# Optimization experiments

Hardware: AMD Instinct MI355X
Metric: run time of the kernel (lower is better)

Reference implementation:

```python
import jax, jax.numpy as jnp
import numpy as np

PAD = 1
K = 3  # kernel_size


def conv2d(x, w, b):
    y = jax.lax.conv_general_dilated(
        x, w, window_strides=(1, 1), padding=((PAD, PAD), (PAD, PAD)),
        dimension_numbers=("NCHW", "OIHW", "NCHW"))
    return y + b[None, :, None, None]


def deform_conv2d(x, offset, weight, bias):
    # torchvision.ops.deform_conv2d semantics (stride=1, dilation=1, 1 offset group)
    B, C, H, W = x.shape
    O = weight.shape[0]
    K2 = K * K
    off = offset.reshape(B, K2, 2, H, W)  # [...,0]=dy, [...,1]=dx
    ky, kx = jnp.meshgrid(jnp.arange(K), jnp.arange(K), indexing="ij")
    ky = ky.reshape(K2).astype(x.dtype)
    kx = kx.reshape(K2).astype(x.dtype)
    hh = jnp.arange(H, dtype=x.dtype)
    ww = jnp.arange(W, dtype=x.dtype)
    # sampling coords, shape [B, K2, H, W]
    py = off[:, :, 0] + ky[None, :, None, None] + hh[None, None, :, None] - PAD
    px = off[:, :, 1] + kx[None, :, None, None] + ww[None, None, None, :] - PAD

    y0 = jnp.floor(py)
    x0 = jnp.floor(px)
    wy = (py - y0)[:, None]  # [B,1,K2,H,W]
    wx = (px - x0)[:, None]

    xf = x.reshape(B, C, H * W)

    def gather(iy, ix):
        valid = (iy >= 0) & (iy < H) & (ix >= 0) & (ix < W)
        iyc = jnp.clip(iy, 0, H - 1).astype(jnp.int32)
        ixc = jnp.clip(ix, 0, W - 1).astype(jnp.int32)
        idx = (iyc * W + ixc).reshape(B, 1, K2 * H * W)
        v = jnp.take_along_axis(xf, idx, axis=2).reshape(B, C, K2, H, W)
        return v * valid.reshape(B, 1, K2, H, W).astype(x.dtype)

    v00 = gather(y0, x0)
    v01 = gather(y0, x0 + 1)
    v10 = gather(y0 + 1, x0)
    v11 = gather(y0 + 1, x0 + 1)
    sampled = (v00 * (1 - wy) * (1 - wx) + v01 * (1 - wy) * wx
               + v10 * wy * (1 - wx) + v11 * wy * wx)  # [B,C,K2,H,W]
    out = jnp.einsum("bckhw,ock->bohw", sampled, weight.reshape(O, C, K2))
    return out + bias[None, :, None, None]


def setup_inputs() -> dict:
    key = jax.random.key(0)
    k1, k2, k3, k4, k5 = jax.random.split(key, 5)
    B, C, H, W = 4, 64, 192, 192
    O = 64
    x = jax.random.normal(k1, (B, C, H, W), dtype=jnp.float32)
    w_off = jax.random.normal(k2, (2 * K * K, C, K, K), dtype=jnp.float32) * 0.05
    b_off = jnp.zeros((2 * K * K,), dtype=jnp.float32)
    w_conv = jax.random.normal(k3, (O, C, K, K), dtype=jnp.float32) * (1.0 / np.sqrt(C * K * K))
    b_conv = jax.random.normal(k4, (O,), dtype=jnp.float32) * 0.01
    return {"x": x, "w_off": w_off, "b_off": b_off, "w_conv": w_conv, "b_conv": b_conv}


def reference(x, w_off, b_off, w_conv, b_conv):
    offset = conv2d(x, w_off, b_off)
    y = deform_conv2d(x, offset, w_conv, b_conv)
    return conv2d(y, w_conv, b_conv)  # module reuses self.conv on deform output
```

## Files before the change

### kernel.cpp

```cpp
#include <hip/hip_runtime.h>

constexpr int B = 4;
constexpr int C = 64;
constexpr int O = 64;
constexpr int OOFF = 18;
constexpr int H = 192;
constexpr int W = 192;

typedef __attribute__((ext_vector_type(8))) short short8;
typedef __attribute__((ext_vector_type(4))) float float4v;
typedef __attribute__((ext_vector_type(2))) float f32x2;
typedef __attribute__((ext_vector_type(2))) uint u32x2;
typedef __attribute__((ext_vector_type(2))) __bf16 bf16x2;

__device__ inline ushort f2bf(float f) {
  return __builtin_bit_cast(ushort, (__bf16)f);
}
__device__ inline uint pk2bf(float lo, float hi) {
  bf16x2 v;
  v.x = (__bf16)lo;
  v.y = (__bf16)hi;
  return __builtin_bit_cast(uint, v);
}
__device__ inline f32x2 upk(uint u) {
  u32x2 t;
  t.x = u << 16;
  t.y = u & 0xffff0000u;
  return __builtin_bit_cast(f32x2, t);
}

__global__ __launch_bounds__(256) void k_pre(const float* __restrict__ x,
                                             ushort* __restrict__ xtb,
                                             const float* __restrict__ w_conv,
                                             ushort* __restrict__ wBf,
                                             const float* __restrict__ w_off,
                                             ushort* __restrict__ wOf) {
  __shared__ float tile[64][17];
  const int bid = blockIdx.x;
  const int tid = threadIdx.x;
  if (bid < 9216) {
    const int w0 = (bid % 12) * 16;
    const int h = (bid / 12) % 192;
    const int b = bid / 2304;
    const int wl = tid & 15;
    const int c0 = tid >> 4;
#pragma unroll
    for (int r = 0; r < 4; ++r) {
      const int c = c0 + r * 16;
      tile[c][wl] = x[(((size_t)b * C + c) * H + h) * W + w0 + wl];
    }
    __syncthreads();
    const int c = tid & 63;
    const int qq = tid >> 6;
#pragma unroll
    for (int r = 0; r < 4; ++r) {
      const int wq = qq + r * 4;
      xtb[(((size_t)b * H + h) * W + w0 + wq) * C + c] = f2bf(tile[c][wq]);
    }
  } else if (bid < 9360) {
    const int i = (bid - 9216) * 256 + tid;
    const int j = i & 7;
    const int lane = (i >> 3) & 63;
    const int nt = (i >> 9) & 3;
    const int kstep = (i >> 11) & 1;
    const int kk = i >> 12;
    const int n = nt + 4 * (lane & 15);
    const int c = kstep * 32 + ((lane >> 4) & 3) * 8 + j;
    wBf[i] = f2bf(w_conv[((size_t)n * C + c) * 9 + kk]);
  } else {
    const int i = (bid - 9360) * 256 + tid;
    const int j = i & 7;
    const int lane = (i >> 3) & 63;
    const int nt = (i >> 9) & 1;
    const int ks = (i >> 10) & 1;
    const int kk = i >> 11;
    const int n = nt * 16 + (lane & 15);
    const int c = ks * 32 + ((lane >> 4) & 3) * 8 + j;
    wOf[i] = (n < OOFF) ? f2bf(w_off[((size_t)n * C + c) * 9 + kk]) : (ushort)0;
  }
}

__global__ __launch_bounds__(256) void k_conv_off_mfma(
    const ushort* __restrict__ xtb, const ushort* __restrict__ wOf,
    const float* __restrict__ b_off, float* __restrict__ offp) {
  const int w0 = blockIdx.x * 16;
  const int b = blockIdx.z;
  const int tid = threadIdx.x;
  const int wave = tid >> 6, lane = tid & 63;
  const int col = lane & 15, quad = lane >> 4;
  const int h0 = blockIdx.y * 8 + wave * 2;

  float4v acc[2][2];
#pragma unroll
  for (int mt = 0; mt < 2; ++mt)
#pragma unroll
    for (int nt = 0; nt < 2; ++nt) acc[mt][nt] = (float4v){0.f, 0.f, 0.f, 0.f};

  short8 bfr[2][2][2];
  short8 afr[2][2][2];

  auto load = [&](int kk, int pb) {
    const int ky = kk / 3, kx = kk % 3;
    const int ww = w0 + col + kx - 1;
    const bool wok = (unsigned)ww < (unsigned)W;
    const int wwc = min(max(ww, 0), W - 1);
#pragma unroll
    for (int ks = 0; ks < 2; ++ks)
#pragma unroll
      for (int nt = 0; nt < 2; ++nt)
        bfr[pb][ks][nt] = *(const short8*)&wOf[((((size_t)kk * 2 + ks) * 2 + nt) * 64 + lane) * 8];
#pragma unroll
    for (int mt = 0; mt < 2; ++mt) {
      const int hh = h0 + mt + ky - 1;
      const bool ok = wok && ((unsigned)hh < (unsigned)H);
      const int hhc = min(max(hh, 0), H - 1);
      const ushort* pa = xtb + (((size_t)b * H + hhc) * W + wwc) * C + quad * 8;
#pragma unroll
      for (int ks = 0; ks < 2; ++ks) {
        short8 v = (short8)0;
        if (ok) v = *(const short8*)(pa + ks * 32);
        afr[pb][mt][ks] = v;
      }
    }
  };

  load(0, 0);
#pragma unroll
  for (int kk = 0; kk < 9; ++kk) {
    const int pb = kk & 1;
    if (kk < 8) load(kk + 1, pb ^ 1);
#pragma unroll
    for (int ks = 0; ks < 2; ++ks)
#pragma unroll
      for (int mt = 0; mt < 2; ++mt)
#pragma unroll
        for (int nt = 0; nt < 2; ++nt)
          acc[mt][nt] = __builtin_amdgcn_mfma_f32_16x16x32_bf16(afr[pb][mt][ks], bfr[pb][ks][nt],
                                                                acc[mt][nt], 0, 0, 0);
  }

#pragma unroll
  for (int mt = 0; mt < 2; ++mt) {
    const int h = h0 + mt;
#pragma unroll
    for (int nt = 0; nt < 2; ++nt) {
      const int o = nt * 16 + col;
      if (o < OOFF) {
        const float bias = b_off[o];
#pragma unroll
        for (int r = 0; r < 4; ++r) {
          const int w = w0 + quad * 4 + r;
          offp[(((size_t)b * H + h) * W + w) * OOFF + o] = acc[mt][nt][r] + bias;
        }
      }
    }
  }
}

__global__ __launch_bounds__(256, 3) void k_deform_mfma(
    const ushort* __restrict__ xtb, const float* __restrict__ offp,
    const ushort* __restrict__ wBf, const float* __restrict__ b_conv,
    ushort* __restrict__ yt) {
  __shared__ ushort sA[2][2][4][64][8];

  const int bid = blockIdx.x;
  const int xcd = bid & 7;
  const int s = bid >> 3;
  const int b = xcd >> 1;
  const int half = xcd & 1;
  const int th = half * 12 + s / 24;
  const int tw = s % 24;
  const int h0 = th * 8, w0 = tw * 8;

  const int tid = threadIdx.x;
  const int wave = tid >> 6, lane = tid & 63;
  const int p = tid >> 2, qtr = tid & 3;
  const int prow = p >> 3, pcol = p & 7;
  const int h = h0 + prow, w = w0 + pcol;
  const int ks_w = qtr >> 1;
  const int q2 = (qtr & 1) * 2;

  const float* po = offp + ((size_t)(b * H + h) * W + w) * OOFF;
  float2 offv[9];
#pragma unroll
  for (int kk = 0; kk < 9; ++kk) offv[kk] = *(const float2*)(po + 2 * kk);

  const ushort* xb = xtb + (size_t)b * H * W * C + qtr * 16;

  uint4 G[2][8];
  float4 aw[2];

  auto issue = [&](int kk, int buf) {
    const float dy = offv[kk].x, dx = offv[kk].y;
    const int ky = kk / 3, kx = kk % 3;
    const float pyf = dy + (float)(ky + h - 1);
    const float pxf = dx + (float)(kx + w - 1);
    const float fy0 = floorf(pyf), fx0 = floorf(pxf);
    const float wy = pyf - fy0, wx = pxf - fx0;
    const int iy0 = (int)fy0, ix0 = (int)fx0;
    const int iy1 = iy0 + 1, ix1 = ix0 + 1;
    const bool vy0 = (unsigned)iy0 < (unsigned)H;
    const bool vy1 = (unsigned)iy1 < (unsigned)H;
    const bool vx0 = (unsigned)ix0 < (unsigned)W;
    const bool vx1 = (unsigned)ix1 < (unsigned)W;
    aw[buf].x = (vy0 && vx0) ? (1.f - wy) * (1.f - wx) : 0.f;
    aw[buf].y = (vy0 && vx1) ? (1.f - wy) * wx : 0.f;
    aw[buf].z = (vy1 && vx0) ? wy * (1.f - wx) : 0.f;
    aw[buf].w = (vy1 && vx1) ? wy * wx : 0.f;
    const int cy0 = min(max(iy0, 0), H - 1), cy1 = min(max(iy1, 0), H - 1);
    const int cx0 = min(max(ix0, 0), W - 1), cx1 = min(max(ix1, 0), W - 1);
    const uint4* p00 = (const uint4*)(xb + ((size_t)cy0 * W + cx0) * C);
    const uint4* p01 = (const uint4*)(xb + ((size_t)cy0 * W + cx1) * C);
    const uint4* p10 = (const uint4*)(xb + ((size_t)cy1 * W + cx0) * C);
    const uint4* p11 = (const uint4*)(xb + ((size_t)cy1 * W + cx1) * C);
    G[buf][0] = p00[0]; G[buf][1] = p00[1];
    G[buf][2] = p01[0]; G[buf][3] = p01[1];
    G[buf][4] = p10[0]; G[buf][5] = p10[1];
    G[buf][6] = p11[0]; G[buf][7] = p11[1];
  };

  float4v acc[4];
#pragma unroll
  for (int nt = 0; nt < 4; ++nt) acc[nt] = (float4v){0.f, 0.f, 0.f, 0.f};

  issue(0, 0);
#pragma unroll
  for (int kk = 0; kk < 9; ++kk) {
    const int buf = kk & 1;
    if (kk < 8) issue(kk + 1, buf ^ 1);

    const f32x2 a00 = {aw[buf].x, aw[buf].x};
    const f32x2 a01 = {aw[buf].y, aw[buf].y};
    const f32x2 a10 = {aw[buf].z, aw[buf].z};
    const f32x2 a11 = {aw[buf].w, aw[buf].w};
    uint pk[8];
#pragma unroll
    for (int i = 0; i < 8; ++i) {
      const uint u00 = ((const uint*)&G[buf][0])[i];
      const uint u01 = ((const uint*)&G[buf][2])[i];
      const uint u10 = ((const uint*)&G[buf][4])[i];
      const uint u11 = ((const uint*)&G[buf][6])[i];
      f32x2 sv = upk(u00) * a00 + upk(u01) * a01 + upk(u10) * a10 + upk(u11) * a11;
      pk[i] = pk2bf(sv.x, sv.y);
    }
    *(uint4*)&sA[buf][ks_w][p >> 4][(p & 15) | (q2 << 4)][0] = *(const uint4*)&pk[0];
    *(uint4*)&sA[buf][ks_w][p >> 4][(p & 15) | ((q2 + 1) << 4)][0] = *(const uint4*)&pk[4];
    __syncthreads();

#pragma unroll
    for (int ks = 0; ks < 2; ++ks) {
      const short8 a = *(const short8*)&sA[buf][ks][wave][lane][0];
#pragma unroll
      for (int nt = 0; nt < 4; ++nt) {
        const short8 bb = *(const short8*)&wBf[((((size_t)kk * 2 + ks) * 4 + nt) * 64 + lane) * 8];
        acc[nt] = __builtin_amdgcn_mfma_f32_16x16x32_bf16(a, bb, acc[nt], 0, 0, 0);
      }
    }
  }

  const int quad = lane >> 4, c16 = lane & 15;
  float bias[4];
#pragma unroll
  for (int nt = 0; nt < 4; ++nt) bias[nt] = b_conv[4 * c16 + nt];
#pragma unroll
  for (int r = 0; r < 4; ++r) {
    const int pp = wave * 16 + quad * 4 + r;
    const int hrow = h0 + (pp >> 3), wcol = w0 + (pp & 7);
    uint2 u;
    u.x = pk2bf(acc[0][r] + bias[0], acc[1][r] + bias[1]);
    u.y = pk2bf(acc[2][r] + bias[2], acc[3][r] + bias[3]);
    *(uint2*)&yt[((size_t)(b * H + hrow) * W + wcol) * C + 4 * c16] = u;
  }
}

__global__ __launch_bounds__(256) void k_conv_main_mfma(
    const ushort* __restrict__ yt, const ushort* __restrict__ wBf,
    const float* __restrict__ b_conv, float* __restrict__ out) {
  const int w0 = blockIdx.x * 16;
  const int b = blockIdx.z;
  const int tid = threadIdx.x;
  const int wave = tid >> 6, lane = tid & 63;
  const int col = lane & 15, quad = lane >> 4;
  const int h0 = blockIdx.y * 8 + wave * 2;

  float4v acc[2][4];
#pragma unroll
  for (int mt = 0; mt < 2; ++mt)
#pragma unroll
    for (int nt = 0; nt < 4; ++nt) acc[mt][nt] = (float4v){0.f, 0.f, 0.f, 0.f};

  short8 bfr[2][2][4];
  short8 afr[2][2][2];

  auto load = [&](int kk, int pb) {
    const int ky = kk / 3, kx = kk % 3;
    const int ww = w0 + col + kx - 1;
    const bool wok = (unsigned)ww < (unsigned)W;
    const int wwc = min(max(ww, 0), W - 1);
#pragma unroll
    for (int ks = 0; ks < 2; ++ks)
#pragma unroll
      for (int nt = 0; nt < 4; ++nt)
        bfr[pb][ks][nt] = *(const short8*)&wBf[((((size_t)kk * 2 + ks) * 4 + nt) * 64 + lane) * 8];
#pragma unroll
    for (int mt = 0; mt < 2; ++mt) {
      const int hh = h0 + mt + ky - 1;
      const bool ok = wok && ((unsigned)hh < (unsigned)H);
      const int hhc = min(max(hh, 0), H - 1);
      const ushort* pa = yt + (((size_t)b * H + hhc) * W + wwc) * C + quad * 8;
#pragma unroll
      for (int ks = 0; ks < 2; ++ks) {
        short8 v = (short8)0;
        if (ok) v = *(const short8*)(pa + ks * 32);
        afr[pb][mt][ks] = v;
      }
    }
  };

  load(0, 0);
#pragma unroll
  for (int kk = 0; kk < 9; ++kk) {
    const int pb = kk & 1;
    if (kk < 8) load(kk + 1, pb ^ 1);
#pragma unroll
    for (int ks = 0; ks < 2; ++ks)
#pragma unroll
      for (int mt = 0; mt < 2; ++mt)
#pragma unroll
        for (int nt = 0; nt < 4; ++nt)
          acc[mt][nt] = __builtin_amdgcn_mfma_f32_16x16x32_bf16(afr[pb][mt][ks], bfr[pb][ks][nt],
                                                                acc[mt][nt], 0, 0, 0);
  }

  float bias[4];
#pragma unroll
  for (int nt = 0; nt < 4; ++nt) bias[nt] = b_conv[4 * col + nt];
#pragma unroll
  for (int mt = 0; mt < 2; ++mt) {
    const int h = h0 + mt;
#pragma unroll
    for (int nt = 0; nt < 4; ++nt) {
      const int oc = 4 * col + nt;
      float4 v;
      v.x = acc[mt][nt][0] + bias[nt];
      v.y = acc[mt][nt][1] + bias[nt];
      v.z = acc[mt][nt][2] + bias[nt];
      v.w = acc[mt][nt][3] + bias[nt];
      *(float4*)&out[(((size_t)b * O + oc) * H + h) * W + w0 + quad * 4] = v;
    }
  }
}

extern "C" void kernel_launch(void* const* d_in, const int* in_sizes, int n_in,
                              void* d_out, int out_size, void* d_ws, size_t ws_size,
                              hipStream_t stream) {
  const float* x = (const float*)d_in[0];
  const float* w_off = (const float*)d_in[1];
  const float* b_off = (const float*)d_in[2];
  const float* w_conv = (const float*)d_in[3];
  const float* b_conv = (const float*)d_in[4];
  float* out = (float*)d_out;

  float* offp = (float*)d_ws;
  ushort* xtb = (ushort*)(offp + (size_t)B * H * W * OOFF);
  ushort* yt = xtb + (size_t)B * H * W * C;
  ushort* wBf = yt + (size_t)B * H * W * C;
  ushort* wOf = wBf + 36864;

  const dim3 blk(256);
  k_pre<<<dim3(9432), blk, 0, stream>>>(x, xtb, w_conv, wBf, w_off, wOf);
  k_conv_off_mfma<<<dim3(W / 16, H / 8, B), blk, 0, stream>>>(xtb, wOf, b_off, offp);
  k_deform_mfma<<<dim3(2304), blk, 0, stream>>>(xtb, offp, wBf, b_conv, yt);
  k_conv_main_mfma<<<dim3(W / 16, H / 8, B), blk, 0, stream>>>(yt, wBf, b_conv, out);
}
```

Measured before the change: 209.8 us.

## Fuse offset convolution into deformable conv kernel via shared-memory offsets

After: 197.6 us. 5.8% less time.

```diff
diff --git a/kernel.cpp b/kernel.cpp
--- a/kernel.cpp
+++ b/kernel.cpp
@@ -80,88 +80,12 @@
   }
 }
 
-__global__ __launch_bounds__(256) void k_conv_off_mfma(
+__global__ __launch_bounds__(256) void k_fused(
     const ushort* __restrict__ xtb, const ushort* __restrict__ wOf,
-    const float* __restrict__ b_off, float* __restrict__ offp) {
-  const int w0 = blockIdx.x * 16;
-  const int b = blockIdx.z;
-  const int tid = threadIdx.x;
-  const int wave = tid >> 6, lane = tid & 63;
-  const int col = lane & 15, quad = lane >> 4;
-  const int h0 = blockIdx.y * 8 + wave * 2;
-
-  float4v acc[2][2];
-#pragma unroll
-  for (int mt = 0; mt < 2; ++mt)
-#pragma unroll
-    for (int nt = 0; nt < 2; ++nt) acc[mt][nt] = (float4v){0.f, 0.f, 0.f, 0.f};
-
-  short8 bfr[2][2][2];
-  short8 afr[2][2][2];
-
-  auto load = [&](int kk, int pb) {
-    const int ky = kk / 3, kx = kk % 3;
-    const int ww = w0 + col + kx - 1;
-    const bool wok = (unsigned)ww < (unsigned)W;
-    const int wwc = min(max(ww, 0), W - 1);
-#pragma unroll
-    for (int ks = 0; ks < 2; ++ks)
-#pragma unroll
-      for (int nt = 0; nt < 2; ++nt)
-        bfr[pb][ks][nt] = *(const short8*)&wOf[((((size_t)kk * 2 + ks) * 2 + nt) * 64 + lane) * 8];
-#pragma unroll
-    for (int mt = 0; mt < 2; ++mt) {
-      const int hh = h0 + mt + ky - 1;
-      const bool ok = wok && ((unsigned)hh < (unsigned)H);
-      const int hhc = min(max(hh, 0), H - 1);
-      const ushort* pa = xtb + (((size_t)b * H + hhc) * W + wwc) * C + quad * 8;
-#pragma unroll
-      for (int ks = 0; ks < 2; ++ks) {
-        short8 v = (short8)0;
-        if (ok) v = *(const short8*)(pa + ks * 32);
-        afr[pb][mt][ks] = v;
-      }
-    }
-  };
-
-  load(0, 0);
-#pragma unroll
-  for (int kk = 0; kk < 9; ++kk) {
-    const int pb = kk & 1;
-    if (kk < 8) load(kk + 1, pb ^ 1);
-#pragma unroll
-    for (int ks = 0; ks < 2; ++ks)
-#pragma unroll
-      for (int mt = 0; mt < 2; ++mt)
-#pragma unroll
-        for (int nt = 0; nt < 2; ++nt)
-          acc[mt][nt] = __builtin_amdgcn_mfma_f32_16x16x32_bf16(afr[pb][mt][ks], bfr[pb][ks][nt],
-                                                                acc[mt][nt], 0, 0, 0);
-  }
-
-#pragma unroll
-  for (int mt = 0; mt < 2; ++mt) {
-    const int h = h0 + mt;
-#pragma unroll
-    for (int nt = 0; nt < 2; ++nt) {
-      const int o = nt * 16 + col;
-      if (o < OOFF) {
-        const float bias = b_off[o];
-#pragma unroll
-        for (int r = 0; r < 4; ++r) {
-          const int w = w0 + quad * 4 + r;
-          offp[(((size_t)b * H + h) * W + w) * OOFF + o] = acc[mt][nt][r] + bias;
-        }
-      }
-    }
-  }
-}
-
-__global__ __launch_bounds__(256, 3) void k_deform_mfma(
-    const ushort* __restrict__ xtb, const float* __restrict__ offp,
-    const ushort* __restrict__ wBf, const float* __restrict__ b_conv,
-    ushort* __restrict__ yt) {
-  __shared__ ushort sA[2][2][4][64][8];
+    const float* __restrict__ b_off, const ushort* __restrict__ wBf,
+    const float* __restrict__ b_conv, ushort* __restrict__ yt) {
+  __shared__ ushort sA[4][2][64][8];
+  __shared__ __align__(16) float offBuf[4][16][20];
 
   const int bid = blockIdx.x;
   const int xcd = bid & 7;
@@ -174,16 +98,65 @@
 
   const int tid = threadIdx.x;
   const int wave = tid >> 6, lane = tid & 63;
+  const int col = lane & 15, quad = lane >> 4;
   const int p = tid >> 2, qtr = tid & 3;
+  const int pl = p & 15;
   const int prow = p >> 3, pcol = p & 7;
   const int h = h0 + prow, w = w0 + pcol;
   const int ks_w = qtr >> 1;
   const int q2 = (qtr & 1) * 2;
 
-  const float* po = offp + ((size_t)(b * H + h) * W + w) * OOFF;
-  float2 offv[9];
-#pragma unroll
-  for (int kk = 0; kk < 9; ++kk) offv[kk] = *(const float2*)(po + 2 * kk);
+  {
+    float4v oacc[2];
+#pragma unroll
+    for (int nt = 0; nt < 2; ++nt) oacc[nt] = (float4v){0.f, 0.f, 0.f, 0.f};
+
+    short8 obfr[2][2][2];
+    short8 oafr[2][2];
+
+    auto oload = [&](int kk, int pb) {
+      const int ky = kk / 3, kx = kk % 3;
+      const int hh = h0 + 2 * wave + (col >> 3) + ky - 1;
+      const int ww = w0 + (col & 7) + kx - 1;
+      const bool ok = ((unsigned)hh < (unsigned)H) && ((unsigned)ww < (unsigned)W);
+      const int hhc = min(max(hh, 0), H - 1);
+      const int wwc = min(max(ww, 0), W - 1);
+      const ushort* pa = xtb + (((size_t)b * H + hhc) * W + wwc) * C + quad * 8;
+#pragma unroll
+      for (int ks = 0; ks < 2; ++ks) {
+        short8 v = (short8)0;
+        if (ok) v = *(const short8*)(pa + ks * 32);
+        oafr[pb][ks] = v;
+#pragma unroll
+        for (int nt = 0; nt < 2; ++nt)
+          obfr[pb][ks][nt] = *(const short8*)&wOf[((((size_t)kk * 2 + ks) * 2 + nt) * 64 + lane) * 8];
+      }
+    };
+
+    oload(0, 0);
+#pragma unroll
+    for (int kk = 0; kk < 9; ++kk) {
+      const int pb = kk & 1;
+      if (kk < 8) oload(kk + 1, pb ^ 1);
+#pragma unroll
+      for (int ks = 0; ks < 2; ++ks)
+#pragma unroll
+        for (int nt = 0; nt < 2; ++nt)
+          oacc[nt] = __builtin_amdgcn_mfma_f32_16x16x32_bf16(oafr[pb][ks], obfr[pb][ks][nt],
+                                                             oacc[nt], 0, 0, 0);
+    }
+
+#pragma unroll
+    for (int nt = 0; nt < 2; ++nt) {
+      const int oc = nt * 16 + col;
+      if (oc < OOFF) {
+        const float bias = b_off[oc];
+#pragma unroll
+        for (int r = 0; r < 4; ++r)
+          offBuf[wave][quad * 4 + r][oc] = oacc[nt][r] + bias;
+      }
+    }
+  }
 
   const ushort* xb = xtb + (size_t)b * H * W * C + qtr * 16;
 
@@ -191,7 +164,8 @@
   float4 aw[2];
 
   auto issue = [&](int kk, int buf) {
-    const float dy = offv[kk].x, dx = offv[kk].y;
+    const float2 ov = *(const float2*)&offBuf[wave][pl][2 * kk];
+    const float dy = ov.x, dx = ov.y;
     const int ky = kk / 3, kx = kk % 3;
     const float pyf = dy + (float)(ky + h - 1);
     const float pxf = dx + (float)(kx + w - 1);
@@ -243,13 +217,12 @@
       f32x2 sv = upk(u00) * a00 + upk(u01) * a01 + upk(u10) * a10 + upk(u11) * a11;
       pk[i] = pk2bf(sv.x, sv.y);
     }
-    *(uint4*)&sA[buf][ks_w][p >> 4][(p & 15) | (q2 << 4)][0] = *(const uint4*)&pk[0];
-    *(uint4*)&sA[buf][ks_w][p >> 4][(p & 15) | ((q2 + 1) << 4)][0] = *(const uint4*)&pk[4];
-    __syncthreads();
+    *(uint4*)&sA[wave][ks_w][pl | (q2 << 4)][0] = *(const uint4*)&pk[0];
+    *(uint4*)&sA[wave][ks_w][pl | ((q2 + 1) << 4)][0] = *(const uint4*)&pk[4];
 
 #pragma unroll
     for (int ks = 0; ks < 2; ++ks) {
-      const short8 a = *(const short8*)&sA[buf][ks][wave][lane][0];
+      const short8 a = *(const short8*)&sA[wave][ks][lane][0];
 #pragma unroll
       for (int nt = 0; nt < 4; ++nt) {
         const short8 bb = *(const short8*)&wBf[((((size_t)kk * 2 + ks) * 4 + nt) * 64 + lane) * 8];
@@ -258,10 +231,9 @@
     }
   }
 
-  const int quad = lane >> 4, c16 = lane & 15;
   float bias[4];
 #pragma unroll
-  for (int nt = 0; nt < 4; ++nt) bias[nt] = b_conv[4 * c16 + nt];
+  for (int nt = 0; nt < 4; ++nt) bias[nt] = b_conv[4 * col + nt];
 #pragma unroll
   for (int r = 0; r < 4; ++r) {
     const int pp = wave * 16 + quad * 4 + r;
@@ -269,7 +241,7 @@
     uint2 u;
     u.x = pk2bf(acc[0][r] + bias[0], acc[1][r] + bias[1]);
     u.y = pk2bf(acc[2][r] + bias[2], acc[3][r] + bias[3]);
-    *(uint2*)&yt[((size_t)(b * H + hrow) * W + wcol) * C + 4 * c16] = u;
+    *(uint2*)&yt[((size_t)(b * H + hrow) * W + wcol) * C + 4 * col] = u;
   }
 }
 
@@ -361,15 +333,13 @@
   const float* b_conv = (const float*)d_in[4];
   float* out = (float*)d_out;
 
-  float* offp = (float*)d_ws;
-  ushort* xtb = (ushort*)(offp + (size_t)B * H * W * OOFF);
+  ushort* xtb = (ushort*)d_ws;
   ushort* yt = xtb + (size_t)B * H * W * C;
   ushort* wBf = yt + (size_t)B * H * W * C;
   ushort* wOf = wBf + 36864;
 
   const dim3 blk(256);
   k_pre<<<dim3(9432), blk, 0, stream>>>(x, xtb, w_conv, wBf, w_off, wOf);
-  k_conv_off_mfma<<<dim3(W / 16, H / 8, B), blk, 0, stream>>>(xtb, wOf, b_off, offp);
-  k_deform_mfma<<<dim3(2304), blk, 0, stream>>>(xtb, offp, wBf, b_conv, yt);
+  k_fused<<<dim3(2304), blk, 0, stream>>>(xtb, wOf, b_off, wBf, b_conv, yt);
   k_conv_main_mfma<<<dim3(W / 16, H / 8, B), blk, 0, stream>>>(yt, wBf, b_conv, out);
 }
```
